# Kernel optimization log

Hardware: AMD Instinct MI355X
Metric: run time of the kernel (lower is better)

Reference implementation:

```python
import jax, jax.numpy as jnp
import numpy as np

N_NODES = 100000

def gcn_conv(x, edge_index, W, b):
    # normalize=False GCNConv: out[i] = sum_{(j->i) in E} (x W)[j] + b
    h = x @ W                                   # [N, out_dim]
    src, dst = edge_index[0], edge_index[1]
    msgs = h[src]                               # [E, out_dim]
    agg = jax.ops.segment_sum(msgs, dst, num_segments=N_NODES)
    return agg + b

def setup_inputs() -> dict:
    key = jax.random.key(0)
    k1, k2, k3, k4 = jax.random.split(key, 4)
    x = jax.random.normal(k1, (N_NODES, 512), dtype=jnp.float32)
    edge_index = jax.random.randint(k2, (2, 3200000), 0, N_NODES, dtype=jnp.int64)
    W1 = jax.random.normal(k3, (512, 16), dtype=jnp.float32) * (1.0 / np.sqrt(512))
    b1 = jnp.zeros((16,), dtype=jnp.float32)
    W2 = jax.random.normal(k4, (16, 40), dtype=jnp.float32) * (1.0 / np.sqrt(16))
    b2 = jnp.zeros((40,), dtype=jnp.float32)
    return {"x": x, "edge_index": edge_index, "W1": W1, "b1": b1, "W2": W2, "b2": b2}

def reference(x, edge_index, W1, b1, W2, b2):
    h = jax.nn.relu(gcn_conv(x, edge_index, W1, b1))
    # dropout is identity at inference (training=False)
    out = gcn_conv(h, edge_index, W2, b2)
    return jax.nn.log_softmax(out, axis=1)
```

## Files before the change

### kernel.cpp

```cpp
#include <hip/hip_runtime.h>
#include <math.h>

#define N_NODES 100000
#define N_EDGES 3200000
#define BSHIFT 7
#define BNODES 128
#define NB 782
#define PLACE_BLOCKS 400

__global__ __launch_bounds__(256) void gemm1_kernel(
    const float* __restrict__ x, const float* __restrict__ W1,
    float* __restrict__ h, int nrows)
{
    const int t   = threadIdx.x;
    const int row = blockIdx.x * 64 + (t >> 2);
    const int cg  = t & 3;
    if (row >= nrows) return;

    const float4* w4 = (const float4*)W1;
    const float4* xr = (const float4*)(x + (size_t)row * 512);

    float4 acc = make_float4(0.f, 0.f, 0.f, 0.f);

    for (int kc4 = 0; kc4 < 128; kc4 += 4) {
        float4 a = xr[kc4 + cg];
        #pragma unroll
        for (int g = 0; g < 4; ++g) {
            float4 v;
            v.x = __shfl(a.x, g, 4);
            v.y = __shfl(a.y, g, 4);
            v.z = __shfl(a.z, g, 4);
            v.w = __shfl(a.w, g, 4);
            const int kb = (kc4 + g) * 4;
            float4 w0 = w4[(kb + 0) * 4 + cg];
            float4 w1 = w4[(kb + 1) * 4 + cg];
            float4 w2 = w4[(kb + 2) * 4 + cg];
            float4 w3 = w4[(kb + 3) * 4 + cg];
            acc.x += v.x * w0.x; acc.y += v.x * w0.y;
            acc.z += v.x * w0.z; acc.w += v.x * w0.w;
            acc.x += v.y * w1.x; acc.y += v.y * w1.y;
            acc.z += v.y * w1.z; acc.w += v.y * w1.w;
            acc.x += v.z * w2.x; acc.y += v.z * w2.y;
            acc.z += v.z * w2.z; acc.w += v.z * w2.w;
            acc.x += v.w * w3.x; acc.y += v.w * w3.y;
            acc.z += v.w * w3.z; acc.w += v.w * w3.w;
        }
    }

    *(float4*)(h + (size_t)row * 16 + cg * 4) = acc;
}

__global__ __launch_bounds__(256) void bin_count_kernel(
    const int* __restrict__ ei, int* __restrict__ bucket_cnt)
{
    __shared__ int hist[NB];
    const int t = threadIdx.x;
    for (int i = t; i < NB; i += 256) hist[i] = 0;
    __syncthreads();
    const int stride = gridDim.x * 256;
    for (int e = blockIdx.x * 256 + t; e < N_EDGES; e += stride)
        atomicAdd(&hist[ei[N_EDGES + e] >> BSHIFT], 1);
    __syncthreads();
    for (int i = t; i < NB; i += 256)
        if (hist[i]) atomicAdd(&bucket_cnt[i], hist[i]);
}

__global__ __launch_bounds__(1024) void bucket_scan_kernel(
    const int* __restrict__ bucket_cnt, int* __restrict__ bucket_base,
    int* __restrict__ bucket_cursor)
{
    __shared__ int s[1024];
    const int t = threadIdx.x;
    s[t] = (t < NB) ? bucket_cnt[t] : 0;
    __syncthreads();
    for (int off = 1; off < 1024; off <<= 1) {
        int v = (t >= off) ? s[t - off] : 0;
        __syncthreads();
        s[t] += v;
        __syncthreads();
    }
    if (t < NB) {
        int excl = (t == 0) ? 0 : s[t - 1];
        bucket_base[t]   = excl;
        bucket_cursor[t] = excl;
        if (t == NB - 1) bucket_base[NB] = s[t];
    }
}

__global__ __launch_bounds__(256) void bin_place_kernel(
    const int* __restrict__ ei, int* __restrict__ bucket_cursor,
    int* __restrict__ packed)
{
    __shared__ int cnt[NB];
    __shared__ int base_off[NB];
    __shared__ int cur[NB];
    const int t = threadIdx.x;
    const int chunk = (N_EDGES + PLACE_BLOCKS - 1) / PLACE_BLOCKS;
    const int cs = blockIdx.x * chunk;
    const int ce = min(cs + chunk, N_EDGES);

    for (int i = t; i < NB; i += 256) { cnt[i] = 0; cur[i] = 0; }
    __syncthreads();
    for (int e = cs + t; e < ce; e += 256)
        atomicAdd(&cnt[ei[N_EDGES + e] >> BSHIFT], 1);
    __syncthreads();
    for (int i = t; i < NB; i += 256)
        base_off[i] = cnt[i] ? atomicAdd(&bucket_cursor[i], cnt[i]) : 0;
    __syncthreads();
    for (int e = cs + t; e < ce; e += 256) {
        int s = ei[e];
        int d = ei[N_EDGES + e];
        int b = d >> BSHIFT;
        int pos = base_off[b] + atomicAdd(&cur[b], 1);
        packed[pos] = s | ((d & (BNODES - 1)) << 17);
    }
}

__global__ __launch_bounds__(256) void csr_sort_kernel(
    const int* __restrict__ bucket_base, const int* __restrict__ packed,
    int* __restrict__ csr_src, int* __restrict__ row_ptr)
{
    __shared__ int hist[BNODES];
    __shared__ int excl[BNODES];
    __shared__ int cur[BNODES];
    __shared__ int scan[BNODES];
    const int t = threadIdx.x;
    const int b = blockIdx.x;
    if (t < BNODES) { hist[t] = 0; cur[t] = 0; }
    __syncthreads();

    const int bs = bucket_base[b];
    const int be = bucket_base[b + 1];
    for (int e = bs + t; e < be; e += 256)
        atomicAdd(&hist[packed[e] >> 17], 1);
    __syncthreads();

    if (t < BNODES) scan[t] = hist[t];
    __syncthreads();
    for (int off = 1; off < BNODES; off <<= 1) {
        int v = (t < BNODES && t >= off) ? scan[t - off] : 0;
        __syncthreads();
        if (t < BNODES) scan[t] += v;
        __syncthreads();
    }
    if (t < BNODES) {
        int ex = (t == 0) ? 0 : scan[t - 1];
        excl[t] = ex;
        int g = b * BNODES + t;
        if (g < N_NODES) row_ptr[g] = bs + ex;
    }
    if (b == NB - 1 && t == 0) row_ptr[N_NODES] = N_EDGES;
    __syncthreads();

    for (int e = bs + t; e < be; e += 256) {
        int p  = packed[e];
        int dl = p >> 17;
        int pos = bs + excl[dl] + atomicAdd(&cur[dl], 1);
        csr_src[pos] = p & 0x1FFFF;
    }
}

__global__ __launch_bounds__(256) void gather1_kernel(
    const int* __restrict__ row_ptr, const int* __restrict__ csr_src,
    const float* __restrict__ h, const float* __restrict__ b1,
    float* __restrict__ h1)
{
    const int node = (blockIdx.x * 256 + threadIdx.x) >> 6;
    if (node >= N_NODES) return;
    const int lane = threadIdx.x & 63;
    const int c = lane & 15, slot = lane >> 4;
    const int start = row_ptr[node], end = row_ptr[node + 1];

    float acc = 0.f;
    int e = start;
    for (; e + 16 <= end; e += 16) {
        int s0 = csr_src[e + slot * 4 + 0];
        int s1 = csr_src[e + slot * 4 + 1];
        int s2 = csr_src[e + slot * 4 + 2];
        int s3 = csr_src[e + slot * 4 + 3];
        float v0 = h[s0 * 16 + c];
        float v1 = h[s1 * 16 + c];
        float v2 = h[s2 * 16 + c];
        float v3 = h[s3 * 16 + c];
        acc += (v0 + v1) + (v2 + v3);
    }
    for (; e + 4 <= end; e += 4)
        acc += h[csr_src[e + slot] * 16 + c];
    if (e + slot < end)
        acc += h[csr_src[e + slot] * 16 + c];

    acc += __shfl_xor(acc, 16);
    acc += __shfl_xor(acc, 32);
    if (lane < 16)
        h1[(size_t)node * 16 + c] = fmaxf(acc + b1[c], 0.f);
}

__global__ __launch_bounds__(256) void gather2_kernel(
    const int* __restrict__ row_ptr, const int* __restrict__ csr_src,
    const float* __restrict__ h1, const float* __restrict__ W2,
    const float* __restrict__ b2, float* __restrict__ out)
{
    const int node = (blockIdx.x * 256 + threadIdx.x) >> 6;
    if (node >= N_NODES) return;
    const int lane = threadIdx.x & 63;
    const int c = lane & 15, slot = lane >> 4;

    float w2c[16];
    float b2v = 0.f;
    if (lane < 40) {
        b2v = b2[lane];
        #pragma unroll
        for (int k = 0; k < 16; ++k) w2c[k] = W2[k * 40 + lane];
    } else {
        #pragma unroll
        for (int k = 0; k < 16; ++k) w2c[k] = 0.f;
    }

    const int start = row_ptr[node], end = row_ptr[node + 1];
    float acc = 0.f;
    int e = start;
    for (; e + 16 <= end; e += 16) {
        int s0 = csr_src[e + slot * 4 + 0];
        int s1 = csr_src[e + slot * 4 + 1];
        int s2 = csr_src[e + slot * 4 + 2];
        int s3 = csr_src[e + slot * 4 + 3];
        float v0 = h1[s0 * 16 + c];
        float v1 = h1[s1 * 16 + c];
        float v2 = h1[s2 * 16 + c];
        float v3 = h1[s3 * 16 + c];
        acc += (v0 + v1) + (v2 + v3);
    }
    for (; e + 4 <= end; e += 4)
        acc += h1[csr_src[e + slot] * 16 + c];
    if (e + slot < end)
        acc += h1[csr_src[e + slot] * 16 + c];

    acc += __shfl_xor(acc, 16);
    acc += __shfl_xor(acc, 32);

    float z = b2v;
    #pragma unroll
    for (int k = 0; k < 16; ++k)
        z += __shfl(acc, k) * w2c[k];

    float zm = (lane < 40) ? z : -1e30f;
    #pragma unroll
    for (int off = 1; off < 64; off <<= 1)
        zm = fmaxf(zm, __shfl_xor(zm, off));
    float ex = (lane < 40) ? __expf(z - zm) : 0.f;
    float sum = ex;
    #pragma unroll
    for (int off = 1; off < 64; off <<= 1)
        sum += __shfl_xor(sum, off);
    const float lse = zm + __logf(sum);

    if (lane < 40)
        out[(size_t)node * 40 + lane] = z - lse;
}

extern "C" void kernel_launch(void* const* d_in, const int* in_sizes, int n_in,
                              void* d_out, int out_size, void* d_ws, size_t ws_size,
                              hipStream_t stream)
{
    const float* x  = (const float*)d_in[0];
    const int*   ei = (const int*)d_in[1];
    const float* W1 = (const float*)d_in[2];
    const float* b1 = (const float*)d_in[3];
    const float* W2 = (const float*)d_in[4];
    const float* b2 = (const float*)d_in[5];
    float* out = (float*)d_out;

    float* h      = (float*)d_ws;
    int*   csr    = (int*)(h + (size_t)N_NODES * 16);
    int*   packed = csr + N_EDGES;
    float* h1     = (float*)packed;
    int*   rowp   = packed + N_EDGES;
    int*   bcnt   = rowp + (N_NODES + 1);
    int*   bbase  = bcnt + NB;
    int*   bcur   = bbase + (NB + 1);

    const int gemm1_blocks  = (N_NODES + 63) / 64;
    const int gather_blocks = (N_NODES + 3) / 4;

    hipMemsetAsync(bcnt, 0, NB * sizeof(int), stream);
    bin_count_kernel  <<<256, 256, 0, stream>>>(ei, bcnt);
    bucket_scan_kernel<<<1, 1024, 0, stream>>>(bcnt, bbase, bcur);
    bin_place_kernel  <<<PLACE_BLOCKS, 256, 0, stream>>>(ei, bcur, packed);
    csr_sort_kernel   <<<NB, 256, 0, stream>>>(bbase, packed, csr, rowp);

    gemm1_kernel<<<gemm1_blocks, 256, 0, stream>>>(x, W1, h, N_NODES);

    gather1_kernel<<<gather_blocks, 256, 0, stream>>>(rowp, csr, h, b1, h1);
    gather2_kernel<<<gather_blocks, 256, 0, stream>>>(rowp, csr, h1, W2, b2, out);
}
```

Baseline: 640.7 us.

## Compute each GEMM1 row in one thread with double-buffered x loads

The x@W1 kernel now assigns one full output row (16 columns) to each thread instead of four threads per row with shuffles. Each thread streams its 512-float x row in 32-float chunks, double-buffered in registers, and reads W1 with uniform addresses that can become scalar loads. This drops the cross-lane shuffles and the per-lane W1 vector loads. In exchange, each thread's x reads are strided by 2 KB across lanes, so global loads coalesce poorly, and register pressure rises, which may lower occupancy. Only 391 blocks are launched.

```diff
diff --git a/kernel.cpp b/kernel.cpp
--- a/kernel.cpp
+++ b/kernel.cpp
@@ -12,42 +12,46 @@
     const float* __restrict__ x, const float* __restrict__ W1,
     float* __restrict__ h, int nrows)
 {
-    const int t   = threadIdx.x;
-    const int row = blockIdx.x * 64 + (t >> 2);
-    const int cg  = t & 3;
+    const int row = blockIdx.x * 256 + threadIdx.x;
     if (row >= nrows) return;
-
-    const float4* w4 = (const float4*)W1;
-    const float4* xr = (const float4*)(x + (size_t)row * 512);
-
-    float4 acc = make_float4(0.f, 0.f, 0.f, 0.f);
-
-    for (int kc4 = 0; kc4 < 128; kc4 += 4) {
-        float4 a = xr[kc4 + cg];
+    const float4* __restrict__ xr = (const float4*)(x + (size_t)row * 512);
+
+    float acc[16];
+    #pragma unroll
+    for (int c = 0; c < 16; ++c) acc[c] = 0.f;
+
+    float4 buf0[8], buf1[8];
+    #pragma unroll
+    for (int i = 0; i < 8; ++i) buf0[i] = xr[i];
+
+    #pragma unroll 2
+    for (int s = 0; s < 16; ++s) {
+        float4* cur = (s & 1) ? buf1 : buf0;
+        float4* nxt = (s & 1) ? buf0 : buf1;
+        if (s < 15) {
+            #pragma unroll
+            for (int i = 0; i < 8; ++i) nxt[i] = xr[(s + 1) * 8 + i];
+        }
         #pragma unroll
-        for (int g = 0; g < 4; ++g) {
-            float4 v;
-            v.x = __shfl(a.x, g, 4);
-            v.y = __shfl(a.y, g, 4);
-            v.z = __shfl(a.z, g, 4);
-            v.w = __shfl(a.w, g, 4);
-            const int kb = (kc4 + g) * 4;
-            float4 w0 = w4[(kb + 0) * 4 + cg];
-            float4 w1 = w4[(kb + 1) * 4 + cg];
-            float4 w2 = w4[(kb + 2) * 4 + cg];
-            float4 w3 = w4[(kb + 3) * 4 + cg];
-            acc.x += v.x * w0.x; acc.y += v.x * w0.y;
-            acc.z += v.x * w0.z; acc.w += v.x * w0.w;
-            acc.x += v.y * w1.x; acc.y += v.y * w1.y;
-            acc.z += v.y * w1.z; acc.w += v.y * w1.w;
-            acc.x += v.z * w2.x; acc.y += v.z * w2.y;
-            acc.z += v.z * w2.z; acc.w += v.z * w2.w;
-            acc.x += v.w * w3.x; acc.y += v.w * w3.y;
-            acc.z += v.w * w3.z; acc.w += v.w * w3.w;
+        for (int i = 0; i < 8; ++i) {
+            const int k0 = s * 32 + i * 4;
+            const float4 xv = cur[i];
+            const float* __restrict__ w0 = W1 + (k0 + 0) * 16;
+            const float* __restrict__ w1 = W1 + (k0 + 1) * 16;
+            const float* __restrict__ w2 = W1 + (k0 + 2) * 16;
+            const float* __restrict__ w3 = W1 + (k0 + 3) * 16;
+            #pragma unroll
+            for (int c = 0; c < 16; ++c)
+                acc[c] += xv.x * w0[c] + xv.y * w1[c]
+                        + xv.z * w2[c] + xv.w * w3[c];
         }
     }
 
-    *(float4*)(h + (size_t)row * 16 + cg * 4) = acc;
+    float4* hp = (float4*)(h + (size_t)row * 16);
+    hp[0] = make_float4(acc[0],  acc[1],  acc[2],  acc[3]);
+    hp[1] = make_float4(acc[4],  acc[5],  acc[6],  acc[7]);
+    hp[2] = make_float4(acc[8],  acc[9],  acc[10], acc[11]);
+    hp[3] = make_float4(acc[12], acc[13], acc[14], acc[15]);
 }
 
 __global__ __launch_bounds__(256) void bin_count_kernel(
@@ -279,7 +283,7 @@
     int*   bbase  = bcnt + NB;
     int*   bcur   = bbase + (NB + 1);
 
-    const int gemm1_blocks  = (N_NODES + 63) / 64;
+    const int gemm1_blocks  = (N_NODES + 255) / 256;
     const int gather_blocks = (N_NODES + 3) / 4;
 
     hipMemsetAsync(bcnt, 0, NB * sizeof(int), stream);
```

Result: slower. 659.6 us (+2.9%).
